# Kernel tuning notes

Measured on AMD Instinct MI355X. Metric: run time of the kernel, lower is better.

## Reference

```python
import jax, jax.numpy as jnp
import numpy as np

RADIUS = 0.45


def _square_distance(src, dst):
    # [B,N,C] x [B,M,C] -> [B,N,M] squared Euclidean distances
    d = -2.0 * jnp.einsum('bnc,bmc->bnm', src, dst)
    d = d + jnp.sum(src * src, -1)[:, :, None]
    d = d + jnp.sum(dst * dst, -1)[:, None, :]
    return d


def _query_ball(radius, nsample, xyz):
    # faithful to torch query_ball_point: mark out-of-radius as N, sort, take nsample, fill with first
    B, N, _ = xyz.shape
    sqr = _square_distance(xyz, xyz)  # [B,N,N]
    idx = jnp.where(sqr > radius * radius, N,
                    jnp.arange(N, dtype=jnp.int32)[None, None, :])
    idx = jnp.sort(idx, axis=-1)[:, :, :nsample]  # [B,N,nsample]
    first = idx[:, :, :1]
    return jnp.where(idx == N, first, idx)


def _gather(points, idx):
    # points [B,N,C], idx [B,S,K] -> [B,S,K,C]
    B = points.shape[0]
    return points[jnp.arange(B)[:, None, None], idx]


def _mlp2(g, W1, b1, W2, b2):
    # g: [B,S,K,Cin]; 1x1 conv2d == per-point matmul; relu each layer
    h = jax.nn.relu(jnp.einsum('bskc,oc->bsko', g, W1) + b1)
    h = jax.nn.relu(jnp.einsum('bski,oi->bsko', h, W2) + b2)
    return jnp.max(h, axis=2)  # max over neighbors K -> [B,S,Cout]


def setup_inputs() -> dict:
    key = jax.random.key(0)
    ks = jax.random.split(key, 13)
    B, N = 8, 2048
    s = 0.1
    return {
        'x': jax.random.uniform(ks[0], (B, N, 3), dtype=jnp.float32),
        'W1a': jax.random.normal(ks[1], (32, 3), dtype=jnp.float32) * s,
        'b1a': jnp.zeros((32,), jnp.float32),
        'W2a': jax.random.normal(ks[2], (64, 32), dtype=jnp.float32) * s,
        'b2a': jnp.zeros((64,), jnp.float32),
        'W1b': jax.random.normal(ks[3], (64, 3), dtype=jnp.float32) * s,
        'b1b': jnp.zeros((64,), jnp.float32),
        'W2b': jax.random.normal(ks[4], (128, 64), dtype=jnp.float32) * s,
        'b2b': jnp.zeros((128,), jnp.float32),
        'Wc1': jax.random.normal(ks[5], (64, 3), dtype=jnp.float32) * s,
        'bc1': jnp.zeros((64,), jnp.float32),
        'Wc2': jax.random.normal(ks[6], (256, 128), dtype=jnp.float32) * s,
        'bc2': jnp.zeros((256,), jnp.float32),
    }


def reference(x, W1a, b1a, W2a, b2a, W1b, b1b, W2b, b2b, Wc1, bc1, Wc2, bc2):
    # branch 1: ball query (nsample=64) -> gather -> 1x1 MLP (3->32->64) -> max-pool
    idx1 = _query_ball(RADIUS, 64, x)
    g1 = _mlp2(_gather(x, idx1), W1a, b1a, W2a, b2a)  # [B,N,64]
    g1 = jnp.transpose(g1, (0, 2, 1))                 # [B,64,N]

    # point-wise conv1d 3->64 on raw coords
    xf = jax.nn.relu(jnp.einsum('bnc,oc->bon', x, Wc1) + bc1[None, :, None])
    xf = jnp.concatenate([xf, g1], axis=1)            # [B,128,N]
    xf = jax.nn.relu(jnp.einsum('bcn,oc->bon', xf, Wc2) + bc2[None, :, None])  # [B,256,N]

    # branch 2: ball query (nsample=128) -> gather -> 1x1 MLP (3->64->128) -> max-pool
    idx2 = _query_ball(RADIUS, 128, x)
    g2 = _mlp2(_gather(x, idx2), W1b, b1b, W2b, b2b)  # [B,N,128]
    g2 = jnp.transpose(g2, (0, 2, 1))                 # [B,128,N]

    return jnp.concatenate([xf, g2], axis=1)          # [B,384,N]
```

## Files before the change

### kernel.cpp

```cpp
#include <hip/hip_runtime.h>
#include <hip/hip_fp16.h>
#include <cstdint>

#define NPTS 2048
#define NB 8
#define R2C 0.2025f

__device__ __forceinline__ float fmul(float a, float b) { return __fmul_rn(a, b); }
__device__ __forceinline__ float fadd(float a, float b) { return __fadd_rn(a, b); }

__device__ __forceinline__ uint hmax2u(uint a, uint b) {
    uint r;
    asm volatile("v_pk_max_f16 %0, %1, %2" : "=v"(r) : "v"(a), "v"(b));
    return r;
}
__device__ __forceinline__ float lo_f(uint u) {
    __half h = __ushort_as_half((unsigned short)(u & 0xffff));
    return __half2float(h);
}
__device__ __forceinline__ float hi_f(uint u) {
    __half h = __ushort_as_half((unsigned short)(u >> 16));
    return __half2float(h);
}

__global__ __launch_bounds__(512, 4) void k_features(
    const float* __restrict__ X,
    const float* __restrict__ W1a, const float* __restrict__ b1a,
    const float* __restrict__ W2a, const float* __restrict__ b2a,
    const float* __restrict__ W1b, const float* __restrict__ b1b,
    const float* __restrict__ W2b, const float* __restrict__ b2b,
    const float* __restrict__ Wc1, const float* __restrict__ bc1,
    __half* __restrict__ fa, __half* __restrict__ fb, float* __restrict__ v)
{
    __shared__ float fat[64 * 33];
    __shared__ float fbt[64 * 67];
    int tid = threadIdx.x;
    int q = __builtin_amdgcn_readfirstlane(tid >> 6);
    int lane = tid & 63;
    int pbase = blockIdx.x * 64;
    int p = pbase + lane;
    int b = p >> 11, i = p & 2047;

    float x0 = X[p * 3 + 0], x1 = X[p * 3 + 1], x2 = X[p * 3 + 2];

    float h[64];
#pragma unroll
    for (int o = 0; o < 32; ++o)
        h[o] = fmaxf(0.f, x0 * W1a[o * 3] + x1 * W1a[o * 3 + 1] + x2 * W1a[o * 3 + 2] + b1a[o]);
#pragma unroll
    for (int oo = 0; oo < 8; oo += 2) {
        int o = q * 8 + oo;
        float a0 = b2a[o], a1 = b2a[o + 1];
#pragma unroll
        for (int k = 0; k < 32; ++k) {
            a0 = fmaf(h[k], W2a[o * 32 + k], a0);
            a1 = fmaf(h[k], W2a[(o + 1) * 32 + k], a1);
        }
        __half2 hh = __floats2half2_rn(fmaxf(0.f, a0), fmaxf(0.f, a1));
        fat[lane * 33 + q * 4 + (oo >> 1)] = *(float*)&hh;
    }
#pragma unroll
    for (int o = 0; o < 64; ++o)
        h[o] = fmaxf(0.f, x0 * W1b[o * 3] + x1 * W1b[o * 3 + 1] + x2 * W1b[o * 3 + 2] + b1b[o]);
#pragma unroll
    for (int oo = 0; oo < 16; oo += 2) {
        int o = q * 16 + oo;
        float a0 = b2b[o], a1 = b2b[o + 1];
#pragma unroll
        for (int k = 0; k < 64; ++k) {
            a0 = fmaf(h[k], W2b[o * 64 + k], a0);
            a1 = fmaf(h[k], W2b[(o + 1) * 64 + k], a1);
        }
        __half2 hh = __floats2half2_rn(fmaxf(0.f, a0), fmaxf(0.f, a1));
        fbt[lane * 67 + q * 8 + (oo >> 1)] = *(float*)&hh;
    }
    float* vb = v + (size_t)b * 128 * NPTS + i;
#pragma unroll
    for (int oo = 0; oo < 8; ++oo) {
        int o = q * 8 + oo;
        vb[(size_t)o * NPTS] =
            fmaxf(0.f, x0 * Wc1[o * 3] + x1 * Wc1[o * 3 + 1] + x2 * Wc1[o * 3 + 2] + bc1[o]);
    }
    __syncthreads();

    uint* fau = (uint*)fa;
#pragma unroll
    for (int r = 0; r < 4; ++r) {
        int idx = r * 512 + tid;
        int pt = idx >> 5, j = idx & 31;
        fau[((size_t)(pbase + pt)) * 32 + j] = *(uint*)&fat[pt * 33 + j];
    }
    uint* fbu = (uint*)fb;
#pragma unroll
    for (int r = 0; r < 8; ++r) {
        int idx = r * 512 + tid;
        int pt = idx >> 6, j = idx & 63;
        fbu[((size_t)(pbase + pt)) * 64 + j] = *(uint*)&fbt[pt * 67 + j];
    }
}

__global__ __launch_bounds__(1024) void k_ballot(
    const float* __restrict__ X, unsigned short* __restrict__ nbrg,
    int* __restrict__ cnt)
{
    __shared__ float4 xs4[NPTS];
    __shared__ unsigned short nbr[16][128];
    __shared__ int cts[16];
    int tid = threadIdx.x;
    int wid = tid >> 6, lane = tid & 63;
    int b = blockIdx.x & 7;
    int i0 = (blockIdx.x >> 3) * 16;
    int i = i0 + wid;

    const float* Xb = X + (size_t)b * NPTS * 3;
    for (int t = tid; t < NPTS; t += 1024) {
        float y0 = Xb[3 * t], y1 = Xb[3 * t + 1], y2 = Xb[3 * t + 2];
        float mm = fadd(fadd(fmul(y0, y0), fmul(y1, y1)), fmul(y2, y2));
        xs4[t] = make_float4(y0, y1, y2, mm);
    }
    __syncthreads();

    float4 cc = xs4[i];
    float n0 = cc.x, n1 = cc.y, n2 = cc.z, nn = cc.w;

    unsigned long long myword = 0;
    for (int w = 0; w < 32; ++w) {
        float4 y = xs4[(w << 6) | lane];
        float dot = fadd(fadd(fmul(n0, y.x), fmul(n1, y.y)), fmul(n2, y.z));
        float d   = fadd(fadd(fmul(-2.0f, dot), nn), y.w);
        unsigned long long bm = __ballot(!(d > R2C));
        if (lane == w) myword = bm;
    }

    int c = (lane < 32) ? __popcll(myword) : 0;
    int incl = c;
#pragma unroll
    for (int d = 1; d < 32; d <<= 1) {
        int t = __shfl_up(incl, d, 64);
        if (lane >= d) incl += t;
    }
    int pre = incl - c;
    if (lane < 32 && c && pre < 128) {
        unsigned long long word = myword;
        int r = pre;
        while (word && r < 128) {
            int pb = __builtin_ctzll(word);
            word &= word - 1;
            nbr[wid][r++] = (unsigned short)((lane << 6) | pb);
        }
    }
    int total = __shfl(incl, 31, 64);
    if (lane == 0) cts[wid] = total;
    __syncthreads();

    uint* ng = (uint*)(nbrg + ((size_t)b * NPTS + i0) * 128);
    ng[tid] = *(uint*)&nbr[tid >> 6][(tid & 63) * 2];
    if (tid < 16) cnt[(size_t)b * NPTS + i0 + tid] = cts[tid];
}

__global__ __launch_bounds__(512, 4) void k_pool(
    const __half* __restrict__ fa, const __half* __restrict__ fb,
    const unsigned short* __restrict__ nbrg, const int* __restrict__ cnt,
    float* __restrict__ v, float* __restrict__ out)
{
    __shared__ uint nbrl[8][64];
    __shared__ float g1t[64][9];
    __shared__ float g2t[128][9];
    int tid = threadIdx.x;
    int wid = __builtin_amdgcn_readfirstlane(tid >> 6);
    int lane = tid & 63;
    int b = blockIdx.x & 7;
    int i0 = (blockIdx.x >> 3) * 8;
    int i = i0 + wid;

    nbrl[tid >> 6][tid & 63] = ((const uint*)(nbrg + ((size_t)b * NPTS + i0) * 128))[tid];
    int total = max(cnt[(size_t)b * NPTS + i], 1);
    int c1 = min(total, 64), c2 = min(total, 128);
    __syncthreads();

    const unsigned short* list = (const unsigned short*)nbrl[wid];

    {
        const uint4* fab = (const uint4*)(fa + (size_t)b * NPTS * 64);
        int g = lane >> 3, c8 = lane & 7;
        int cl = c1 - 1;
        uint4 r[8];
#pragma unroll
        for (int j = 0; j < 8; ++j) {
            int idx = j * 8 + g; idx = idx > cl ? cl : idx;
            r[j] = fab[(int)list[idx] * 8 + c8];
        }
        uint acc0 = 0, acc1 = 0, acc2 = 0, acc3 = 0;
#pragma unroll
        for (int j = 0; j < 8; ++j) {
            acc0 = hmax2u(acc0, r[j].x);
            acc1 = hmax2u(acc1, r[j].y);
            acc2 = hmax2u(acc2, r[j].z);
            acc3 = hmax2u(acc3, r[j].w);
        }
#pragma unroll
        for (int s = 8; s < 64; s <<= 1) {
            acc0 = hmax2u(acc0, (uint)__shfl_xor((int)acc0, s, 64));
            acc1 = hmax2u(acc1, (uint)__shfl_xor((int)acc1, s, 64));
            acc2 = hmax2u(acc2, (uint)__shfl_xor((int)acc2, s, 64));
            acc3 = hmax2u(acc3, (uint)__shfl_xor((int)acc3, s, 64));
        }
        if (g == 0) {
            uint a[4] = {acc0, acc1, acc2, acc3};
#pragma unroll
            for (int k = 0; k < 4; ++k) {
                g1t[8 * c8 + 2 * k][wid]     = lo_f(a[k]);
                g1t[8 * c8 + 2 * k + 1][wid] = hi_f(a[k]);
            }
        }
    }
    {
        const uint4* fbb = (const uint4*)(fb + (size_t)b * NPTS * 128);
        int g = lane >> 4, c8 = lane & 15;
        int cl = c2 - 1;
        uint acc0 = 0, acc1 = 0, acc2 = 0, acc3 = 0;
#pragma unroll
        for (int jo = 0; jo < 32; jo += 16) {
            uint4 r[16];
#pragma unroll
            for (int jj = 0; jj < 16; ++jj) {
                int idx = (jo + jj) * 4 + g; idx = idx > cl ? cl : idx;
                r[jj] = fbb[(int)list[idx] * 16 + c8];
            }
#pragma unroll
            for (int jj = 0; jj < 16; ++jj) {
                acc0 = hmax2u(acc0, r[jj].x);
                acc1 = hmax2u(acc1, r[jj].y);
                acc2 = hmax2u(acc2, r[jj].z);
                acc3 = hmax2u(acc3, r[jj].w);
            }
        }
#pragma unroll
        for (int s = 16; s < 64; s <<= 1) {
            acc0 = hmax2u(acc0, (uint)__shfl_xor((int)acc0, s, 64));
            acc1 = hmax2u(acc1, (uint)__shfl_xor((int)acc1, s, 64));
            acc2 = hmax2u(acc2, (uint)__shfl_xor((int)acc2, s, 64));
            acc3 = hmax2u(acc3, (uint)__shfl_xor((int)acc3, s, 64));
        }
        if (g == 0) {
            uint a[4] = {acc0, acc1, acc2, acc3};
#pragma unroll
            for (int k = 0; k < 4; ++k) {
                g2t[8 * c8 + 2 * k][wid]     = lo_f(a[k]);
                g2t[8 * c8 + 2 * k + 1][wid] = hi_f(a[k]);
            }
        }
    }
    __syncthreads();

    {
        int ch = tid >> 3, pt = tid & 7;
        v[((size_t)b * 128 + 64 + ch) * NPTS + i0 + pt] = g1t[ch][pt];
    }
#pragma unroll
    for (int r = 0; r < 2; ++r) {
        int idx = r * 512 + tid;
        int ch = idx >> 3, pt = idx & 7;
        out[((size_t)b * 384 + 256 + ch) * NPTS + i0 + pt] = g2t[ch][pt];
    }
}

__global__ __launch_bounds__(256) void k_conv2(
    const float* __restrict__ v, const float* __restrict__ Wc2,
    const float* __restrict__ bc2, float* __restrict__ out)
{
    __shared__ float vs[128 * 32];
    __shared__ float ws[256 * 33];
    int b = blockIdx.x & 7;
    int nt = (blockIdx.x >> 3) << 5;
    int t = threadIdx.x;
    int n_t = t & 3, o_t = t >> 2;

    const float* vb = v + (size_t)b * 128 * NPTS + nt;
#pragma unroll
    for (int r = 0; r < 4; ++r) {
        int j = r * 256 + t; int k = j >> 3, n4 = j & 7;
        *(float4*)&vs[k * 32 + n4 * 4] = *(const float4*)(vb + (size_t)k * NPTS + n4 * 4);
    }

    float acc[4][8];
#pragma unroll
    for (int r = 0; r < 4; ++r) {
        float bb = bc2[o_t * 4 + r];
#pragma unroll
        for (int n = 0; n < 8; ++n) acc[r][n] = bb;
    }

    for (int kc = 0; kc < 128; kc += 32) {
        __syncthreads();
#pragma unroll
        for (int r = 0; r < 8; ++r) {
            int j = r * 256 + t; int o = j >> 3, c = j & 7;
            float4 wv = *(const float4*)(Wc2 + (size_t)o * 128 + kc + c * 4);
            ws[o * 33 + c * 4 + 0] = wv.x;
            ws[o * 33 + c * 4 + 1] = wv.y;
            ws[o * 33 + c * 4 + 2] = wv.z;
            ws[o * 33 + c * 4 + 3] = wv.w;
        }
        __syncthreads();
#pragma unroll 4
        for (int kk = 0; kk < 32; ++kk) {
            float4 va = *(float4*)&vs[(kc + kk) * 32 + n_t * 8];
            float4 vb4 = *(float4*)&vs[(kc + kk) * 32 + n_t * 8 + 4];
            float vv[8] = {va.x, va.y, va.z, va.w, vb4.x, vb4.y, vb4.z, vb4.w};
            float ww[4];
#pragma unroll
            for (int r = 0; r < 4; ++r) ww[r] = ws[(o_t * 4 + r) * 33 + kk];
#pragma unroll
            for (int r = 0; r < 4; ++r)
#pragma unroll
                for (int n = 0; n < 8; ++n)
                    acc[r][n] = fmaf(ww[r], vv[n], acc[r][n]);
        }
    }

    float* ob = out + ((size_t)b * 384 + o_t * 4) * NPTS + nt + n_t * 8;
#pragma unroll
    for (int r = 0; r < 4; ++r) {
        float4 s0, s1;
        s0.x = fmaxf(0.f, acc[r][0]); s0.y = fmaxf(0.f, acc[r][1]);
        s0.z = fmaxf(0.f, acc[r][2]); s0.w = fmaxf(0.f, acc[r][3]);
        s1.x = fmaxf(0.f, acc[r][4]); s1.y = fmaxf(0.f, acc[r][5]);
        s1.z = fmaxf(0.f, acc[r][6]); s1.w = fmaxf(0.f, acc[r][7]);
        *(float4*)(ob + (size_t)r * NPTS) = s0;
        *(float4*)(ob + (size_t)r * NPTS + 4) = s1;
    }
}

extern "C" void kernel_launch(void* const* d_in, const int* in_sizes, int n_in,
                              void* d_out, int out_size, void* d_ws, size_t ws_size,
                              hipStream_t stream) {
    const float* X   = (const float*)d_in[0];
    const float* W1a = (const float*)d_in[1];
    const float* b1a = (const float*)d_in[2];
    const float* W2a = (const float*)d_in[3];
    const float* b2a = (const float*)d_in[4];
    const float* W1b = (const float*)d_in[5];
    const float* b1b = (const float*)d_in[6];
    const float* W2b = (const float*)d_in[7];
    const float* b2b = (const float*)d_in[8];
    const float* Wc1 = (const float*)d_in[9];
    const float* bc1 = (const float*)d_in[10];
    const float* Wc2 = (const float*)d_in[11];
    const float* bc2 = (const float*)d_in[12];
    float* out = (float*)d_out;

    __half* fa = (__half*)d_ws;
    __half* fb = fa + (size_t)NB * NPTS * 64;
    float*  v  = (float*)(fb + (size_t)NB * NPTS * 128);
    unsigned short* nbrg = (unsigned short*)(v + (size_t)NB * 128 * NPTS);
    int* cnt = (int*)(nbrg + (size_t)NB * NPTS * 128);

    k_features<<<NB * NPTS / 64, 512, 0, stream>>>(X, W1a, b1a, W2a, b2a,
                                                   W1b, b1b, W2b, b2b, Wc1, bc1,
                                                   fa, fb, v);
    k_ballot<<<NB * NPTS / 16, 1024, 0, stream>>>(X, nbrg, cnt);
    k_pool<<<NB * NPTS / 8, 512, 0, stream>>>(fa, fb, nbrg, cnt, v, out);
    k_conv2<<<NB * (NPTS / 32), 256, 0, stream>>>(v, Wc2, bc2, out);
}
```

Measured before the change: 178.7 us.

## Fuse ball-query ballot kernel with neighbor max-pool kernel

Merges the ballot-based neighbor search and the gather/max-pool kernel into one kernel with 8 query points per 512-thread block. The neighbor lists stay in shared memory instead of being written to and read back from global memory, which also removes one kernel launch. In exchange, each block now stages all 2048 points of its batch into LDS for only 8 queries. That doubles the redundant coordinate loads and preprocessing, and the larger per-block LDS footprint may limit occupancy.

After: 164.7 us. 7.8% less time.

```diff
diff --git a/kernel.cpp b/kernel.cpp
--- a/kernel.cpp
+++ b/kernel.cpp
@@ -99,21 +99,23 @@
     }
 }
 
-__global__ __launch_bounds__(1024) void k_ballot(
-    const float* __restrict__ X, unsigned short* __restrict__ nbrg,
-    int* __restrict__ cnt)
+__global__ __launch_bounds__(512, 4) void k_query(
+    const float* __restrict__ X, const __half* __restrict__ fa,
+    const __half* __restrict__ fb, float* __restrict__ v, float* __restrict__ out)
 {
     __shared__ float4 xs4[NPTS];
-    __shared__ unsigned short nbr[16][128];
-    __shared__ int cts[16];
+    __shared__ unsigned short nbr[8][128];
+    __shared__ float g1t[64][9];
+    __shared__ float g2t[128][9];
     int tid = threadIdx.x;
-    int wid = tid >> 6, lane = tid & 63;
+    int wid = __builtin_amdgcn_readfirstlane(tid >> 6);
+    int lane = tid & 63;
     int b = blockIdx.x & 7;
-    int i0 = (blockIdx.x >> 3) * 16;
+    int i0 = (blockIdx.x >> 3) * 8;
     int i = i0 + wid;
 
     const float* Xb = X + (size_t)b * NPTS * 3;
-    for (int t = tid; t < NPTS; t += 1024) {
+    for (int t = tid; t < NPTS; t += 512) {
         float y0 = Xb[3 * t], y1 = Xb[3 * t + 1], y2 = Xb[3 * t + 2];
         float mm = fadd(fadd(fmul(y0, y0), fmul(y1, y1)), fmul(y2, y2));
         xs4[t] = make_float4(y0, y1, y2, mm);
@@ -150,35 +152,9 @@
         }
     }
     int total = __shfl(incl, 31, 64);
-    if (lane == 0) cts[wid] = total;
-    __syncthreads();
-
-    uint* ng = (uint*)(nbrg + ((size_t)b * NPTS + i0) * 128);
-    ng[tid] = *(uint*)&nbr[tid >> 6][(tid & 63) * 2];
-    if (tid < 16) cnt[(size_t)b * NPTS + i0 + tid] = cts[tid];
-}
-
-__global__ __launch_bounds__(512, 4) void k_pool(
-    const __half* __restrict__ fa, const __half* __restrict__ fb,
-    const unsigned short* __restrict__ nbrg, const int* __restrict__ cnt,
-    float* __restrict__ v, float* __restrict__ out)
-{
-    __shared__ uint nbrl[8][64];
-    __shared__ float g1t[64][9];
-    __shared__ float g2t[128][9];
-    int tid = threadIdx.x;
-    int wid = __builtin_amdgcn_readfirstlane(tid >> 6);
-    int lane = tid & 63;
-    int b = blockIdx.x & 7;
-    int i0 = (blockIdx.x >> 3) * 8;
-    int i = i0 + wid;
-
-    nbrl[tid >> 6][tid & 63] = ((const uint*)(nbrg + ((size_t)b * NPTS + i0) * 128))[tid];
-    int total = max(cnt[(size_t)b * NPTS + i], 1);
     int c1 = min(total, 64), c2 = min(total, 128);
-    __syncthreads();
-
-    const unsigned short* list = (const unsigned short*)nbrl[wid];
+
+    const unsigned short* list = nbr[wid];
 
     {
         const uint4* fab = (const uint4*)(fa + (size_t)b * NPTS * 64);
@@ -353,13 +329,10 @@
     __half* fa = (__half*)d_ws;
     __half* fb = fa + (size_t)NB * NPTS * 64;
     float*  v  = (float*)(fb + (size_t)NB * NPTS * 128);
-    unsigned short* nbrg = (unsigned short*)(v + (size_t)NB * 128 * NPTS);
-    int* cnt = (int*)(nbrg + (size_t)NB * NPTS * 128);
 
     k_features<<<NB * NPTS / 64, 512, 0, stream>>>(X, W1a, b1a, W2a, b2a,
                                                    W1b, b1b, W2b, b2b, Wc1, bc1,
                                                    fa, fb, v);
-    k_ballot<<<NB * NPTS / 16, 1024, 0, stream>>>(X, nbrg, cnt);
-    k_pool<<<NB * NPTS / 8, 512, 0, stream>>>(fa, fb, nbrg, cnt, v, out);
+    k_query<<<NB * NPTS / 8, 512, 0, stream>>>(X, fa, fb, v, out);
     k_conv2<<<NB * (NPTS / 32), 256, 0, stream>>>(v, Wc2, bc2, out);
 }
```
